# Kernel optimization log

Measured on AMD Instinct MI355X. Metric: run time of the kernel, lower is better.

Reference implementation:

```python
import jax, jax.numpy as jnp
import numpy as np

B, S, D, H = 4, 2048, 1024, 16
HD = D // H


def setup_inputs() -> dict:
    key = jax.random.key(0)
    ks = jax.random.split(key, 6)
    scale = 1.0 / np.sqrt(D)
    return {
        'x': jax.random.normal(ks[0], (B, S, D), dtype=jnp.float32),
        'wq': jax.random.normal(ks[1], (D, D), dtype=jnp.float32) * scale,
        'wk': jax.random.normal(ks[2], (D, D), dtype=jnp.float32) * scale,
        'wv': jax.random.normal(ks[3], (D, D), dtype=jnp.float32) * scale,
        'wo': jax.random.normal(ks[4], (D, D), dtype=jnp.float32) * scale,
        'wo_b': jnp.zeros((D,), dtype=jnp.float32),
    }


def reference(x, wq, wk, wv, wo, wo_b):
    b, s, _ = x.shape
    # Linear projections (torch Linear: x @ W.T), reshape to [b, h, s, hd]
    def proj(w):
        return jnp.einsum('bsd,ed->bse', x, w).reshape(b, s, H, HD).transpose(0, 2, 1, 3)
    q, k, v = proj(wq), proj(wk), proj(wv)
    scores = jnp.einsum('bhqd,bhkd->bhqk', q, k)  # [b,h,s,s]
    causal = jnp.triu(jnp.ones((s, s), dtype=bool), k=1)
    scores = jnp.where(causal, -jnp.inf, scores)
    attn = jax.nn.softmax(scores / np.sqrt(HD), axis=-1)
    ctx = jnp.einsum('bhqk,bhkd->bhqd', attn, v)  # [b,h,s,hd]
    ctx = ctx.transpose(0, 2, 1, 3).reshape(b, s, D)
    return jnp.einsum('bsd,ed->bse', ctx, wo) + wo_b
```

## Files before the change

### kernel.cpp

```cpp
#include <hip/hip_runtime.h>

#define SB 4
#define SS 2048
#define SD 1024
#define SH 16
#define SHD 64
#define SM (SB * SS)

typedef __bf16 bf16x8 __attribute__((ext_vector_type(8)));
typedef float f32x4 __attribute__((ext_vector_type(4)));

static __device__ __forceinline__ unsigned short f2bf(float x) {
    unsigned int u = __builtin_bit_cast(unsigned int, x);
    u += 0x7fffu + ((u >> 16) & 1u);
    return (unsigned short)(u >> 16);
}

static __device__ __forceinline__ float fast_exp2(float x) {
#if __has_builtin(__builtin_amdgcn_exp2f)
    return __builtin_amdgcn_exp2f(x);
#else
    return exp2f(x);
#endif
}

static __device__ __forceinline__ unsigned int pkhi(float a, float b) {
    return __builtin_amdgcn_perm(__builtin_bit_cast(unsigned int, a),
                                 __builtin_bit_cast(unsigned int, b), 0x07060302u);
}

typedef __attribute__((address_space(1))) void GV;
typedef __attribute__((address_space(3))) void LV;

static __device__ __forceinline__ void async16(const void* g, void* l) {
    __builtin_amdgcn_global_load_lds((GV*)g, (LV*)l, 16, 0, 0);
}

#define QSCALE 0.18033688011112042f

__global__ __launch_bounds__(256) void cast_all(
    const float* __restrict__ x,  const float* __restrict__ wq,
    const float* __restrict__ wk, const float* __restrict__ wv,
    const float* __restrict__ wo,
    unsigned short* __restrict__ xb, unsigned short* __restrict__ wqkv,
    unsigned short* __restrict__ wo16) {
    int base = blockIdx.x * 512 + threadIdx.x;
#pragma unroll
    for (int it = 0; it < 2; ++it) {
        int i = base + it * 256;
        const float4* src;
        ushort4* dst;
        if (i < 2097152) {
            src = reinterpret_cast<const float4*>(x) + i;
            dst = reinterpret_cast<ushort4*>(xb) + i;
        } else {
            int j = i - 2097152;
            int which = j >> 18;
            int r = j & 262143;
            if (which == 0) {
                src = reinterpret_cast<const float4*>(wq) + r;
                dst = reinterpret_cast<ushort4*>(wqkv) + r;
            } else if (which == 1) {
                src = reinterpret_cast<const float4*>(wk) + r;
                dst = reinterpret_cast<ushort4*>(wqkv) + 262144 + r;
            } else if (which == 2) {
                src = reinterpret_cast<const float4*>(wv) + r;
                dst = reinterpret_cast<ushort4*>(wqkv) + 524288 + r;
            } else {
                src = reinterpret_cast<const float4*>(wo) + r;
                dst = reinterpret_cast<ushort4*>(wo16) + r;
            }
        }
        float4 v = *src;
        ushort4 o;
        o.x = f2bf(v.x); o.y = f2bf(v.y); o.z = f2bf(v.z); o.w = f2bf(v.w);
        *dst = o;
    }
}

#define NT16 (SD / 64)

__device__ __forceinline__ void gemm_mainloop(
    const unsigned short* __restrict__ A,
    const unsigned short* __restrict__ Bt,
    int tileM, int tileN, int tid,
    unsigned short* As0, unsigned short* As1, unsigned short* As2,
    unsigned short* Bs0, unsigned short* Bs1,
    f32x4 (&acc)[4][4]) {

    const int lane = tid & 63;
    const int quad = lane >> 4;
    const int col0 = lane & 15;
    const int w = tid >> 6;
    const int wm = w >> 1;
    const int wn = w & 1;

    const int r0 = tid >> 3;
    const int cc = ((tid & 7) ^ (r0 & 7)) * 8;

    const unsigned short* gA0 = A + (size_t)(tileM + r0) * SD + cc;
    const unsigned short* gA1 = gA0 + (size_t)64 * SD;
    const unsigned short* gA2 = gA0 + (size_t)128 * SD;
    const unsigned short* gA3 = gA0 + (size_t)192 * SD;
    const unsigned short* gB0 = Bt + (size_t)(tileN + r0) * SD + cc;
    const unsigned short* gB1 = gB0 + (size_t)64 * SD;

    unsigned short* const Asb[3] = {As0, As1, As2};
    unsigned short* const Bsb[2] = {Bs0, Bs1};
    const int t16 = tid * 16;

    const int cs0 = (quad ^ (col0 & 7)) * 16;
    const int cs1 = ((4 + quad) ^ (col0 & 7)) * 16;
    const int arow = (wm * 64 + col0) * 128;
    const int brow = (wn * 64 + col0) * 128;

#define STAGE_A(t, Asx) do {                                         \
        async16(gA0 + (t) * 64, (char*)(Asx) + t16);                 \
        async16(gA1 + (t) * 64, (char*)(Asx) + 8192 + t16);          \
        async16(gA2 + (t) * 64, (char*)(Asx) + 16384 + t16);         \
        async16(gA3 + (t) * 64, (char*)(Asx) + 24576 + t16);         \
    } while (0)
#define STAGE_B(t, Bsx) do {                                         \
        async16(gB0 + (t) * 64, (char*)(Bsx) + t16);                 \
        async16(gB1 + (t) * 64, (char*)(Bsx) + 8192 + t16);          \
    } while (0)

    STAGE_A(0, As0);
    STAGE_B(0, Bs0);
    STAGE_A(1, As1);

#pragma unroll
    for (int t = 0; t < NT16; ++t) {
        if (t + 1 < NT16)
            asm volatile("s_waitcnt vmcnt(4)" ::: "memory");
        else
            asm volatile("s_waitcnt vmcnt(0)" ::: "memory");
        __builtin_amdgcn_s_barrier();
        __builtin_amdgcn_sched_barrier(0);

        const unsigned short* As = Asb[t % 3];
        const unsigned short* Bs = Bsb[t & 1];

        bf16x8 af[4][2], bfr[4][2];
#pragma unroll
        for (int fr = 0; fr < 4; ++fr) {
            const char* rp = (const char*)As + arow + fr * 2048;
            af[fr][0] = *reinterpret_cast<const bf16x8*>(rp + cs0);
            af[fr][1] = *reinterpret_cast<const bf16x8*>(rp + cs1);
        }
#pragma unroll
        for (int fc = 0; fc < 4; ++fc) {
            const char* rp = (const char*)Bs + brow + fc * 2048;
            bfr[fc][0] = *reinterpret_cast<const bf16x8*>(rp + cs0);
            bfr[fc][1] = *reinterpret_cast<const bf16x8*>(rp + cs1);
        }

        if (t + 1 < NT16) STAGE_B(t + 1, Bsb[(t + 1) & 1]);
        if (t + 2 < NT16) STAGE_A(t + 2, Asb[(t + 2) % 3]);

        __builtin_amdgcn_s_setprio(1);
#pragma unroll
        for (int ks = 0; ks < 2; ++ks)
#pragma unroll
            for (int fr = 0; fr < 4; ++fr)
#pragma unroll
                for (int fc = 0; fc < 4; ++fc)
                    acc[fr][fc] = __builtin_amdgcn_mfma_f32_16x16x32_bf16(
                        af[fr][ks], bfr[fc][ks], acc[fr][fc], 0, 0, 0);
        __builtin_amdgcn_s_setprio(0);
    }
#undef STAGE_A
#undef STAGE_B
}

__global__ __launch_bounds__(512, 2) void gemm_qkv(
    const unsigned short* __restrict__ xb,
    const unsigned short* __restrict__ wqkv,
    unsigned short* __restrict__ Qd,
    unsigned short* __restrict__ Kd,
    unsigned short* __restrict__ Vtd) {

    __shared__ __align__(16) unsigned short As0[256 * 64];
    __shared__ __align__(16) unsigned short As1[256 * 64];
    __shared__ __align__(16) unsigned short As2[256 * 64];
    __shared__ __align__(16) unsigned short Bs0[128 * 64];
    __shared__ __align__(16) unsigned short Bs1[128 * 64];
    const int tid = threadIdx.x;
    const int tileN = blockIdx.x * 128;
    const int tileM = blockIdx.y * 256;

    f32x4 acc[4][4];
    const f32x4 z = {0.f, 0.f, 0.f, 0.f};
#pragma unroll
    for (int i = 0; i < 4; ++i)
#pragma unroll
        for (int j = 0; j < 4; ++j) acc[i][j] = z;

    gemm_mainloop(xb, wqkv, tileM, tileN, tid, As0, As1, As2, Bs0, Bs1, acc);

    const int lane = tid & 63, quad = lane >> 4, col0 = lane & 15;
    const int w = tid >> 6, wm = w >> 1, wn = w & 1;

#pragma unroll
    for (int ct = 0; ct < 4; ++ct) {
        int n0 = tileN + wn * 64 + ct * 16;
        int which = n0 >> 10;
        int e0 = n0 & 1023;
        int h = e0 >> 6;
        int hd = (e0 & 63) + col0;
#pragma unroll
        for (int rt = 0; rt < 4; ++rt) {
            int m0 = tileM + wm * 64 + rt * 16 + quad * 4;
            int bb = m0 >> 11;
            int s0 = m0 & 2047;
            int bh = bb * SH + h;
            if (which == 0) {
                int base = (bh * SS + s0) * SHD + hd;
#pragma unroll
                for (int r = 0; r < 4; ++r)
                    Qd[base + r * SHD] = f2bf(acc[rt][ct][r] * QSCALE);
            } else if (which == 1) {
                int base = (bh * SS + s0) * SHD + hd;
#pragma unroll
                for (int r = 0; r < 4; ++r)
                    Kd[base + r * SHD] = f2bf(acc[rt][ct][r]);
            } else {
                int base = (bh * SHD + hd) * SS + s0;
                ushort4 pk;
                pk.x = f2bf(acc[rt][ct][0]);
                pk.y = f2bf(acc[rt][ct][1]);
                pk.z = f2bf(acc[rt][ct][2]);
                pk.w = f2bf(acc[rt][ct][3]);
                *reinterpret_cast<ushort4*>(Vtd + base) = pk;
            }
        }
    }
}

__global__ __launch_bounds__(512, 2) void gemm_out(
    const unsigned short* __restrict__ ctx,
    const unsigned short* __restrict__ wo16,
    const float* __restrict__ wb,
    float* __restrict__ out) {

    __shared__ __align__(16) unsigned short As0[256 * 64];
    __shared__ __align__(16) unsigned short As1[256 * 64];
    __shared__ __align__(16) unsigned short As2[256 * 64];
    __shared__ __align__(16) unsigned short Bs0[128 * 64];
    __shared__ __align__(16) unsigned short Bs1[128 * 64];
    const int tid = threadIdx.x;
    const int tileN = blockIdx.x * 128;
    const int tileM = blockIdx.y * 256;

    f32x4 acc[4][4];
    const f32x4 z = {0.f, 0.f, 0.f, 0.f};
#pragma unroll
    for (int i = 0; i < 4; ++i)
#pragma unroll
        for (int j = 0; j < 4; ++j) acc[i][j] = z;

    gemm_mainloop(ctx, wo16, tileM, tileN, tid, As0, As1, As2, Bs0, Bs1, acc);

    const int lane = tid & 63, quad = lane >> 4, col0 = lane & 15;
    const int w = tid >> 6, wm = w >> 1, wn = w & 1;

#pragma unroll
    for (int ct = 0; ct < 4; ++ct) {
        int n = tileN + wn * 64 + ct * 16 + col0;
        float bias = wb[n];
#pragma unroll
        for (int rt = 0; rt < 4; ++rt) {
            int m0 = tileM + wm * 64 + rt * 16 + quad * 4;
#pragma unroll
            for (int r = 0; r < 4; ++r)
                out[(size_t)(m0 + r) * SD + n] = acc[rt][ct][r] + bias;
        }
    }
}

#define PSTR 72

__device__ __forceinline__ void stage_kv(
    const unsigned short* __restrict__ Kg,
    const unsigned short* __restrict__ Vtg,
    size_t base, int t, int srow0, int scs, int tid,
    unsigned short* Kb, unsigned short* Vb) {
#pragma unroll
    for (int j = 0; j < 2; ++j) {
        int row = j * 32 + srow0;
        int chunk = scs ^ (row & 7);
        int slot16 = (j * 256 + tid) * 16;
        async16(Kg + base + (size_t)(t * 64 + row) * SHD + chunk * 8,
                (char*)Kb + slot16);
        async16(Vtg + base + (size_t)row * SS + t * 64 + chunk * 8,
                (char*)Vb + slot16);
    }
}

__device__ __forceinline__ void attn_tile(
    const unsigned short* __restrict__ Kc,
    const unsigned short* __restrict__ Vc,
    int kb, int q0, int quad, int col0,
    const bf16x8 (&bq)[2][2], const bf16x8& ones,
    unsigned short* Psw, f32x4 (&ot)[2][4], f32x4 (&lacc)[2]) {

    const f32x4 z = {0.f, 0.f, 0.f, 0.f};

    bf16x8 ak[4][2];
#pragma unroll
    for (int rt = 0; rt < 4; ++rt)
#pragma unroll
        for (int ks = 0; ks < 2; ++ks)
            ak[rt][ks] = *reinterpret_cast<const bf16x8*>(
                &Kc[(rt * 16 + col0) * 64 + ((ks * 4 + quad) ^ (col0 & 7)) * 8]);

    f32x4 sc[2][4];
#pragma unroll
    for (int g = 0; g < 2; ++g)
#pragma unroll
        for (int rt = 0; rt < 4; ++rt) sc[g][rt] = z;
    __builtin_amdgcn_s_setprio(1);
#pragma unroll
    for (int rt = 0; rt < 4; ++rt)
#pragma unroll
        for (int g = 0; g < 2; ++g) {
            sc[g][rt] = __builtin_amdgcn_mfma_f32_16x16x32_bf16(
                ak[rt][0], bq[g][0], sc[g][rt], 0, 0, 0);
            sc[g][rt] = __builtin_amdgcn_mfma_f32_16x16x32_bf16(
                ak[rt][1], bq[g][1], sc[g][rt], 0, 0, 0);
        }
    __builtin_amdgcn_s_setprio(0);

    if (kb + 63 > q0) {
#pragma unroll
        for (int g = 0; g < 2; ++g) {
            int q = q0 + g * 16 + col0;
#pragma unroll
            for (int rt = 0; rt < 4; ++rt)
#pragma unroll
                for (int r = 0; r < 4; ++r) {
                    int key = kb + rt * 16 + quad * 4 + r;
                    if (key > q) sc[g][rt][r] = -3.0e38f;
                }
        }
    }

#pragma unroll
    for (int g = 0; g < 2; ++g)
#pragma unroll
        for (int rt = 0; rt < 4; ++rt)
#pragma unroll
            for (int r = 0; r < 4; ++r)
                sc[g][rt][r] = fast_exp2(sc[g][rt][r]);

    bf16x8 bp[2][2];
#pragma unroll
    for (int g = 0; g < 2; ++g) {
#pragma unroll
        for (int rt = 0; rt < 4; ++rt) {
            uint2 pk;
            pk.x = pkhi(sc[g][rt][1], sc[g][rt][0]);
            pk.y = pkhi(sc[g][rt][3], sc[g][rt][2]);
            *reinterpret_cast<uint2*>(&Psw[col0 * PSTR + rt * 16 + quad * 4]) = pk;
        }
#pragma unroll
        for (int ks = 0; ks < 2; ++ks)
            bp[g][ks] = *reinterpret_cast<const bf16x8*>(
                &Psw[col0 * PSTR + ks * 32 + quad * 8]);
    }

    __builtin_amdgcn_s_setprio(1);
#pragma unroll
    for (int ks = 0; ks < 2; ++ks) {
        lacc[0] = __builtin_amdgcn_mfma_f32_16x16x32_bf16(ones, bp[0][ks], lacc[0], 0, 0, 0);
        lacc[1] = __builtin_amdgcn_mfma_f32_16x16x32_bf16(ones, bp[1][ks], lacc[1], 0, 0, 0);
#pragma unroll
        for (int ct = 0; ct < 4; ++ct) {
            bf16x8 av = *reinterpret_cast<const bf16x8*>(
                &Vc[(ct * 16 + col0) * 64 + ((ks * 4 + quad) ^ (col0 & 7)) * 8]);
            ot[0][ct] = __builtin_amdgcn_mfma_f32_16x16x32_bf16(av, bp[0][ks], ot[0][ct], 0, 0, 0);
            ot[1][ct] = __builtin_amdgcn_mfma_f32_16x16x32_bf16(av, bp[1][ks], ot[1][ct], 0, 0, 0);
        }
    }
    __builtin_amdgcn_s_setprio(0);
}

__device__ __forceinline__ void attn_pass(
    const unsigned short* __restrict__ Qg,
    const unsigned short* __restrict__ Kg,
    const unsigned short* __restrict__ Vtg,
    unsigned short* __restrict__ ctx,
    size_t base, int b, int h, int jj,
    int tid, int w, int quad, int col0,
    unsigned short* K0, unsigned short* K1, unsigned short* K2, unsigned short* K3,
    unsigned short* V0, unsigned short* V1, unsigned short* V2, unsigned short* V3,
    unsigned short* Psw, const bf16x8& ones) {

    const int q0 = jj * 128 + w * 32;
    const int qlim = q0 + 31;

    bf16x8 bq[2][2];
#pragma unroll
    for (int g = 0; g < 2; ++g)
#pragma unroll
        for (int ks = 0; ks < 2; ++ks)
            bq[g][ks] = *reinterpret_cast<const bf16x8*>(
                Qg + base + (size_t)(q0 + g * 16 + col0) * SHD + ks * 32 + quad * 8);

    f32x4 ot[2][4], lacc[2];
    const f32x4 z = {0.f, 0.f, 0.f, 0.f};
#pragma unroll
    for (int g = 0; g < 2; ++g) {
        lacc[g] = z;
#pragma unroll
        for (int ct = 0; ct < 4; ++ct) ot[g][ct] = z;
    }

    const int srow0 = tid >> 3;
    const int scs = tid & 7;
    const int nkt = 2 * jj + 2;

    __syncthreads();
    stage_kv(Kg, Vtg, base, 0, srow0, scs, tid, K0, V0);
    if (1 < nkt) stage_kv(Kg, Vtg, base, 1, srow0, scs, tid, K1, V1);

#pragma unroll 1
    for (int kt = 0; kt < nkt; kt += 4) {
        __syncthreads();
        if (kt + 2 < nkt) stage_kv(Kg, Vtg, base, kt + 2, srow0, scs, tid, K2, V2);
        if (kt + 3 < nkt) stage_kv(Kg, Vtg, base, kt + 3, srow0, scs, tid, K3, V3);
        if (kt * 64 <= qlim)
            attn_tile(K0, V0, kt * 64, q0, quad, col0, bq, ones, Psw, ot, lacc);
        if ((kt + 1) * 64 <= qlim)
            attn_tile(K1, V1, (kt + 1) * 64, q0, quad, col0, bq, ones, Psw, ot, lacc);

        if (kt + 2 >= nkt) break;
        __syncthreads();
        if (kt + 4 < nkt) stage_kv(Kg, Vtg, base, kt + 4, srow0, scs, tid, K0, V0);
        if (kt + 5 < nkt) stage_kv(Kg, Vtg, base, kt + 5, srow0, scs, tid, K1, V1);
        if ((kt + 2) * 64 <= qlim)
            attn_tile(K2, V2, (kt + 2) * 64, q0, quad, col0, bq, ones, Psw, ot, lacc);
        if (kt + 3 < nkt && (kt + 3) * 64 <= qlim)
            attn_tile(K3, V3, (kt + 3) * 64, q0, quad, col0, bq, ones, Psw, ot, lacc);
    }

#pragma unroll
    for (int g = 0; g < 2; ++g) {
        float inv = 1.0f / lacc[g][0];
        int q = q0 + g * 16 + col0;
        size_t obase = ((size_t)b * SS + q) * SD + h * SHD;
#pragma unroll
        for (int ct = 0; ct < 4; ++ct) {
            uint2 pk;
            pk.x = pkhi(ot[g][ct][1] * inv, ot[g][ct][0] * inv);
            pk.y = pkhi(ot[g][ct][3] * inv, ot[g][ct][2] * inv);
            *reinterpret_cast<uint2*>(ctx + obase + ct * 16 + quad * 4) = pk;
        }
    }
}

__global__ __launch_bounds__(256) void attn_kernel(
    const unsigned short* __restrict__ Qg,
    const unsigned short* __restrict__ Kg,
    const unsigned short* __restrict__ Vtg,
    unsigned short* __restrict__ ctx) {

    __shared__ __align__(16) unsigned short K0[64 * 64];
    __shared__ __align__(16) unsigned short K1[64 * 64];
    __shared__ __align__(16) unsigned short K2[64 * 64];
    __shared__ __align__(16) unsigned short K3[64 * 64];
    __shared__ __align__(16) unsigned short V0[64 * 64];
    __shared__ __align__(16) unsigned short V1[64 * 64];
    __shared__ __align__(16) unsigned short V2[64 * 64];
    __shared__ __align__(16) unsigned short V3[64 * 64];
    __shared__ __align__(16) unsigned short Ps[4 * 16 * PSTR];

    const int tid = threadIdx.x;
    const int w = tid >> 6;
    const int lane = tid & 63;
    const int quad = lane >> 4;
    const int col0 = lane & 15;

    const int bh = (blockIdx.x << 3) | (blockIdx.y & 7);
    const int jx = blockIdx.y >> 3;

    const int b = bh >> 4;
    const int h = bh & 15;
    const size_t base = (size_t)bh * (SS * SHD);
    unsigned short* Psw = Ps + w * 16 * PSTR;

    bf16x8 ones;
#pragma unroll
    for (int i = 0; i < 8; ++i) ones[i] = (__bf16)1.0f;

    attn_pass(Qg, Kg, Vtg, ctx, base, b, h, jx,
              tid, w, quad, col0, K0, K1, K2, K3, V0, V1, V2, V3, Psw, ones);
    attn_pass(Qg, Kg, Vtg, ctx, base, b, h, 15 - jx,
              tid, w, quad, col0, K0, K1, K2, K3, V0, V1, V2, V3, Psw, ones);
}

extern "C" void kernel_launch(void* const* d_in, const int* in_sizes, int n_in,
                              void* d_out, int out_size, void* d_ws, size_t ws_size,
                              hipStream_t stream) {
    const float* x  = (const float*)d_in[0];
    const float* wq = (const float*)d_in[1];
    const float* wk = (const float*)d_in[2];
    const float* wv = (const float*)d_in[3];
    const float* wo = (const float*)d_in[4];
    const float* wb = (const float*)d_in[5];
    float* out = (float*)d_out;

    char* ws = (char*)d_ws;
    unsigned short* xb   = (unsigned short*)(ws + 0);
    unsigned short* wqkv = (unsigned short*)(ws + 16777216);
    unsigned short* q    = (unsigned short*)(ws + 23068672);
    unsigned short* k    = (unsigned short*)(ws + 39845888);
    unsigned short* vt   = (unsigned short*)(ws + 56623104);
    unsigned short* ctx  = (unsigned short*)(ws + 73400320);
    unsigned short* wo16 = (unsigned short*)(ws + 90177536);

    cast_all<<<6144, 256, 0, stream>>>(x, wq, wk, wv, wo, xb, wqkv, wo16);

    gemm_qkv<<<dim3(3 * SD / 128, SM / 256), 512, 0, stream>>>(xb, wqkv, q, k, vt);

    attn_kernel<<<dim3(8, SB * SH), 256, 0, stream>>>(q, k, vt, ctx);

    gemm_out<<<dim3(SD / 128, SM / 256), 512, 0, stream>>>(ctx, wo16, wb, out);
}
```

Measured before the change: 234.6 us.

## Merge paired causal query blocks into one K/V sweep sharing staged tiles

Previously each block made two separate passes over K/V, one for the low query block jj and one for the mirrored block 15-jj, and restaged the shared K/V prefix each time. Now a single sweep processes both query blocks together. Each K/V tile is loaded to LDS once and reused for both query sets, with the low block masked off once it is past its causal limit. This halves K/V staging traffic and barriers for the shared prefix, but doubles accumulator registers per thread. The kernel also now asks for 2 blocks per CU through launch_bounds, which may force register spills. Both P tiles are written to the same per-warp Psw buffer, which relies on the B-side LDS write being ordered after the A-side reads.

```diff
diff --git a/kernel.cpp b/kernel.cpp
--- a/kernel.cpp
+++ b/kernel.cpp
@@ -297,44 +297,33 @@
     }
 }
 
-__device__ __forceinline__ void attn_tile(
-    const unsigned short* __restrict__ Kc,
-    const unsigned short* __restrict__ Vc,
-    int kb, int q0, int quad, int col0,
-    const bf16x8 (&bq)[2][2], const bf16x8& ones,
-    unsigned short* Psw, f32x4 (&ot)[2][4], f32x4 (&lacc)[2]) {
+__device__ __forceinline__ void qk_softmax_pair(
+    const bf16x8 (&ak)[4][2], const bf16x8& bq0, const bf16x8& bq1,
+    const bf16x8& bq0b, const bf16x8& bq1b,
+    int kb, int qrow0, int quad, int col0,
+    unsigned short* Psw, bf16x8 (&bp)[2][2]) {
 
     const f32x4 z = {0.f, 0.f, 0.f, 0.f};
-
-    bf16x8 ak[4][2];
-#pragma unroll
-    for (int rt = 0; rt < 4; ++rt)
-#pragma unroll
-        for (int ks = 0; ks < 2; ++ks)
-            ak[rt][ks] = *reinterpret_cast<const bf16x8*>(
-                &Kc[(rt * 16 + col0) * 64 + ((ks * 4 + quad) ^ (col0 & 7)) * 8]);
-
     f32x4 sc[2][4];
 #pragma unroll
     for (int g = 0; g < 2; ++g)
 #pragma unroll
         for (int rt = 0; rt < 4; ++rt) sc[g][rt] = z;
+
     __builtin_amdgcn_s_setprio(1);
 #pragma unroll
-    for (int rt = 0; rt < 4; ++rt)
+    for (int rt = 0; rt < 4; ++rt) {
+        sc[0][rt] = __builtin_amdgcn_mfma_f32_16x16x32_bf16(ak[rt][0], bq0, sc[0][rt], 0, 0, 0);
+        sc[1][rt] = __builtin_amdgcn_mfma_f32_16x16x32_bf16(ak[rt][0], bq0b, sc[1][rt], 0, 0, 0);
+        sc[0][rt] = __builtin_amdgcn_mfma_f32_16x16x32_bf16(ak[rt][1], bq1, sc[0][rt], 0, 0, 0);
+        sc[1][rt] = __builtin_amdgcn_mfma_f32_16x16x32_bf16(ak[rt][1], bq1b, sc[1][rt], 0, 0, 0);
+    }
+    __builtin_amdgcn_s_setprio(0);
+
+    if (kb + 63 > qrow0) {
 #pragma unroll
         for (int g = 0; g < 2; ++g) {
-            sc[g][rt] = __builtin_amdgcn_mfma_f32_16x16x32_bf16(
-                ak[rt][0], bq[g][0], sc[g][rt], 0, 0, 0);
-            sc[g][rt] = __builtin_amdgcn_mfma_f32_16x16x32_bf16(
-                ak[rt][1], bq[g][1], sc[g][rt], 0, 0, 0);
-        }
-    __builtin_amdgcn_s_setprio(0);
-
-    if (kb + 63 > q0) {
-#pragma unroll
-        for (int g = 0; g < 2; ++g) {
-            int q = q0 + g * 16 + col0;
+            int q = qrow0 + g * 16 + col0;
 #pragma unroll
             for (int rt = 0; rt < 4; ++rt)
 #pragma unroll
@@ -353,7 +342,6 @@
             for (int r = 0; r < 4; ++r)
                 sc[g][rt][r] = fast_exp2(sc[g][rt][r]);
 
-    bf16x8 bp[2][2];
 #pragma unroll
     for (int g = 0; g < 2; ++g) {
 #pragma unroll
@@ -368,98 +356,57 @@
             bp[g][ks] = *reinterpret_cast<const bf16x8*>(
                 &Psw[col0 * PSTR + ks * 32 + quad * 8]);
     }
+}
+
+__device__ __forceinline__ void attn_tile9(
+    const unsigned short* __restrict__ Kc,
+    const unsigned short* __restrict__ Vc,
+    int kb, int qlimA, int q0a, int q0b, int quad, int col0,
+    const bf16x8 (&bq)[4][2], const bf16x8& ones,
+    unsigned short* Psw, f32x4 (&ot)[4][4], f32x4 (&lacc)[4]) {
+
+    bf16x8 ak[4][2];
+#pragma unroll
+    for (int rt = 0; rt < 4; ++rt)
+#pragma unroll
+        for (int ks = 0; ks < 2; ++ks)
+            ak[rt][ks] = *reinterpret_cast<const bf16x8*>(
+                &Kc[(rt * 16 + col0) * 64 + ((ks * 4 + quad) ^ (col0 & 7)) * 8]);
+
+    const bool actA = (kb <= qlimA);
+
+    bf16x8 bpA[2][2], bpB[2][2];
+    if (actA)
+        qk_softmax_pair(ak, bq[0][0], bq[0][1], bq[1][0], bq[1][1],
+                        kb, q0a, quad, col0, Psw, bpA);
+    qk_softmax_pair(ak, bq[2][0], bq[2][1], bq[3][0], bq[3][1],
+                    kb, q0b, quad, col0, Psw, bpB);
 
     __builtin_amdgcn_s_setprio(1);
 #pragma unroll
     for (int ks = 0; ks < 2; ++ks) {
-        lacc[0] = __builtin_amdgcn_mfma_f32_16x16x32_bf16(ones, bp[0][ks], lacc[0], 0, 0, 0);
-        lacc[1] = __builtin_amdgcn_mfma_f32_16x16x32_bf16(ones, bp[1][ks], lacc[1], 0, 0, 0);
+        lacc[2] = __builtin_amdgcn_mfma_f32_16x16x32_bf16(ones, bpB[0][ks], lacc[2], 0, 0, 0);
+        lacc[3] = __builtin_amdgcn_mfma_f32_16x16x32_bf16(ones, bpB[1][ks], lacc[3], 0, 0, 0);
+        if (actA) {
+            lacc[0] = __builtin_amdgcn_mfma_f32_16x16x32_bf16(ones, bpA[0][ks], lacc[0], 0, 0, 0);
+            lacc[1] = __builtin_amdgcn_mfma_f32_16x16x32_bf16(ones, bpA[1][ks], lacc[1], 0, 0, 0);
+        }
 #pragma unroll
         for (int ct = 0; ct < 4; ++ct) {
             bf16x8 av = *reinterpret_cast<const bf16x8*>(
                 &Vc[(ct * 16 + col0) * 64 + ((ks * 4 + quad) ^ (col0 & 7)) * 8]);
-            ot[0][ct] = __builtin_amdgcn_mfma_f32_16x16x32_bf16(av, bp[0][ks], ot[0][ct], 0, 0, 0);
-            ot[1][ct] = __builtin_amdgcn_mfma_f32_16x16x32_bf16(av, bp[1][ks], ot[1][ct], 0, 0, 0);
+            ot[2][ct] = __builtin_amdgcn_mfma_f32_16x16x32_bf16(av, bpB[0][ks], ot[2][ct], 0, 0, 0);
+            ot[3][ct] = __builtin_amdgcn_mfma_f32_16x16x32_bf16(av, bpB[1][ks], ot[3][ct], 0, 0, 0);
+            if (actA) {
+                ot[0][ct] = __builtin_amdgcn_mfma_f32_16x16x32_bf16(av, bpA[0][ks], ot[0][ct], 0, 0, 0);
+                ot[1][ct] = __builtin_amdgcn_mfma_f32_16x16x32_bf16(av, bpA[1][ks], ot[1][ct], 0, 0, 0);
+            }
         }
     }
     __builtin_amdgcn_s_setprio(0);
 }
 
-__device__ __forceinline__ void attn_pass(
-    const unsigned short* __restrict__ Qg,
-    const unsigned short* __restrict__ Kg,
-    const unsigned short* __restrict__ Vtg,
-    unsigned short* __restrict__ ctx,
-    size_t base, int b, int h, int jj,
-    int tid, int w, int quad, int col0,
-    unsigned short* K0, unsigned short* K1, unsigned short* K2, unsigned short* K3,
-    unsigned short* V0, unsigned short* V1, unsigned short* V2, unsigned short* V3,
-    unsigned short* Psw, const bf16x8& ones) {
-
-    const int q0 = jj * 128 + w * 32;
-    const int qlim = q0 + 31;
-
-    bf16x8 bq[2][2];
-#pragma unroll
-    for (int g = 0; g < 2; ++g)
-#pragma unroll
-        for (int ks = 0; ks < 2; ++ks)
-            bq[g][ks] = *reinterpret_cast<const bf16x8*>(
-                Qg + base + (size_t)(q0 + g * 16 + col0) * SHD + ks * 32 + quad * 8);
-
-    f32x4 ot[2][4], lacc[2];
-    const f32x4 z = {0.f, 0.f, 0.f, 0.f};
-#pragma unroll
-    for (int g = 0; g < 2; ++g) {
-        lacc[g] = z;
-#pragma unroll
-        for (int ct = 0; ct < 4; ++ct) ot[g][ct] = z;
-    }
-
-    const int srow0 = tid >> 3;
-    const int scs = tid & 7;
-    const int nkt = 2 * jj + 2;
-
-    __syncthreads();
-    stage_kv(Kg, Vtg, base, 0, srow0, scs, tid, K0, V0);
-    if (1 < nkt) stage_kv(Kg, Vtg, base, 1, srow0, scs, tid, K1, V1);
-
-#pragma unroll 1
-    for (int kt = 0; kt < nkt; kt += 4) {
-        __syncthreads();
-        if (kt + 2 < nkt) stage_kv(Kg, Vtg, base, kt + 2, srow0, scs, tid, K2, V2);
-        if (kt + 3 < nkt) stage_kv(Kg, Vtg, base, kt + 3, srow0, scs, tid, K3, V3);
-        if (kt * 64 <= qlim)
-            attn_tile(K0, V0, kt * 64, q0, quad, col0, bq, ones, Psw, ot, lacc);
-        if ((kt + 1) * 64 <= qlim)
-            attn_tile(K1, V1, (kt + 1) * 64, q0, quad, col0, bq, ones, Psw, ot, lacc);
-
-        if (kt + 2 >= nkt) break;
-        __syncthreads();
-        if (kt + 4 < nkt) stage_kv(Kg, Vtg, base, kt + 4, srow0, scs, tid, K0, V0);
-        if (kt + 5 < nkt) stage_kv(Kg, Vtg, base, kt + 5, srow0, scs, tid, K1, V1);
-        if ((kt + 2) * 64 <= qlim)
-            attn_tile(K2, V2, (kt + 2) * 64, q0, quad, col0, bq, ones, Psw, ot, lacc);
-        if (kt + 3 < nkt && (kt + 3) * 64 <= qlim)
-            attn_tile(K3, V3, (kt + 3) * 64, q0, quad, col0, bq, ones, Psw, ot, lacc);
-    }
-
-#pragma unroll
-    for (int g = 0; g < 2; ++g) {
-        float inv = 1.0f / lacc[g][0];
-        int q = q0 + g * 16 + col0;
-        size_t obase = ((size_t)b * SS + q) * SD + h * SHD;
-#pragma unroll
-        for (int ct = 0; ct < 4; ++ct) {
-            uint2 pk;
-            pk.x = pkhi(ot[g][ct][1] * inv, ot[g][ct][0] * inv);
-            pk.y = pkhi(ot[g][ct][3] * inv, ot[g][ct][2] * inv);
-            *reinterpret_cast<uint2*>(ctx + obase + ct * 16 + quad * 4) = pk;
-        }
-    }
-}
-
-__global__ __launch_bounds__(256) void attn_kernel(
+__global__ __launch_bounds__(256, 2) void attn_kernel(
     const unsigned short* __restrict__ Qg,
     const unsigned short* __restrict__ Kg,
     const unsigned short* __restrict__ Vtg,
@@ -482,7 +429,7 @@
     const int col0 = lane & 15;
 
     const int bh = (blockIdx.x << 3) | (blockIdx.y & 7);
-    const int jx = blockIdx.y >> 3;
+    const int jj = blockIdx.y >> 3;
 
     const int b = bh >> 4;
     const int h = bh & 15;
@@ -493,10 +440,74 @@
 #pragma unroll
     for (int i = 0; i < 8; ++i) ones[i] = (__bf16)1.0f;
 
-    attn_pass(Qg, Kg, Vtg, ctx, base, b, h, jx,
-              tid, w, quad, col0, K0, K1, K2, K3, V0, V1, V2, V3, Psw, ones);
-    attn_pass(Qg, Kg, Vtg, ctx, base, b, h, 15 - jx,
-              tid, w, quad, col0, K0, K1, K2, K3, V0, V1, V2, V3, Psw, ones);
+    const int q0a = jj * 128 + w * 32;
+    const int q0b = (15 - jj) * 128 + w * 32;
+    const int qlimA = q0a + 31;
+    const int qlimB = q0b + 31;
+    const int nkt = 32 - 2 * jj;
+
+    bf16x8 bq[4][2];
+#pragma unroll
+    for (int g = 0; g < 4; ++g) {
+        int qr = (g < 2 ? q0a + g * 16 : q0b + (g - 2) * 16) + col0;
+#pragma unroll
+        for (int ks = 0; ks < 2; ++ks)
+            bq[g][ks] = *reinterpret_cast<const bf16x8*>(
+                Qg + base + (size_t)qr * SHD + ks * 32 + quad * 8);
+    }
+
+    f32x4 ot[4][4], lacc[4];
+    const f32x4 z = {0.f, 0.f, 0.f, 0.f};
+#pragma unroll
+    for (int g = 0; g < 4; ++g) {
+        lacc[g] = z;
+#pragma unroll
+        for (int ct = 0; ct < 4; ++ct) ot[g][ct] = z;
+    }
+
+    const int srow0 = tid >> 3;
+    const int scs = tid & 7;
+
+    stage_kv(Kg, Vtg, base, 0, srow0, scs, tid, K0, V0);
+    stage_kv(Kg, Vtg, base, 1, srow0, scs, tid, K1, V1);
+
+#pragma unroll 1
+    for (int kt = 0; kt < nkt; kt += 4) {
+        __syncthreads();
+        if (kt + 2 < nkt) stage_kv(Kg, Vtg, base, kt + 2, srow0, scs, tid, K2, V2);
+        if (kt + 3 < nkt) stage_kv(Kg, Vtg, base, kt + 3, srow0, scs, tid, K3, V3);
+        if (kt * 64 <= qlimB)
+            attn_tile9(K0, V0, kt * 64, qlimA, q0a, q0b, quad, col0,
+                       bq, ones, Psw, ot, lacc);
+        if ((kt + 1) * 64 <= qlimB)
+            attn_tile9(K1, V1, (kt + 1) * 64, qlimA, q0a, q0b, quad, col0,
+                       bq, ones, Psw, ot, lacc);
+
+        if (kt + 2 >= nkt) break;
+        __syncthreads();
+        if (kt + 4 < nkt) stage_kv(Kg, Vtg, base, kt + 4, srow0, scs, tid, K0, V0);
+        if (kt + 5 < nkt) stage_kv(Kg, Vtg, base, kt + 5, srow0, scs, tid, K1, V1);
+        if ((kt + 2) * 64 <= qlimB)
+            attn_tile9(K2, V2, (kt + 2) * 64, qlimA, q0a, q0b, quad, col0,
+                       bq, ones, Psw, ot, lacc);
+        if ((kt + 3) < nkt && (kt + 3) * 64 <= qlimB)
+            attn_tile9(K3, V3, (kt + 3) * 64, qlimA, q0a, q0b, quad, col0,
+                       bq, ones, Psw, ot, lacc);
+    }
+
+#pragma unroll
+    for (int g = 0; g < 4; ++g) {
+        float inv = 1.0f / lacc[g][0];
+        int q = (g < 2 ? q0a + g * 16 : q0b + (g - 2) * 16) + col0;
+        size_t obase = ((size_t)b * SS + q) * SD + h * SHD;
+#pragma unroll
+        for (int ct = 0; ct < 4; ++ct) {
+            uint2 pk;
+            pk.x = pkhi(ot[g][ct][1] * inv, ot[g][ct][0] * inv);
+            pk.y = pkhi(ot[g][ct][3] * inv, ot[g][ct][2] * inv);
+            *reinterpret_cast<uint2*>(ctx + obase + ct * 16 + quad * 4) = pk;
+        }
+    }
 }
 
 extern "C" void kernel_launch(void* const* d_in, const int* in_sizes, int n_in,
```

Measured after the change: 235.2 us. No clear change (+0.3%).

## Split causal attention into one query tile per block with double-buffered K/V

Applied to the files above, without the earlier changes.

The attention kernel now launches twice as many blocks, each handling a single 128-row query tile. Previously each block processed a balanced pair of tiles (jx and 15-jx) in sequence. Tiles are ordered heaviest-first through the j2 = 15 - index mapping, and the K/V staging ring drops from four buffers to two, with one tile prefetched ahead. This roughly halves LDS use per block, which should allow more resident blocks per CU and finer-grained load balancing. The cost is a shallower prefetch pipeline that may expose more global-load latency, plus per-block tail imbalance from causal work varying between tiles.

```diff
diff --git a/kernel.cpp b/kernel.cpp
--- a/kernel.cpp
+++ b/kernel.cpp
@@ -385,19 +385,39 @@
     __builtin_amdgcn_s_setprio(0);
 }
 
-__device__ __forceinline__ void attn_pass(
+__global__ __launch_bounds__(256) void attn_kernel(
     const unsigned short* __restrict__ Qg,
     const unsigned short* __restrict__ Kg,
     const unsigned short* __restrict__ Vtg,
-    unsigned short* __restrict__ ctx,
-    size_t base, int b, int h, int jj,
-    int tid, int w, int quad, int col0,
-    unsigned short* K0, unsigned short* K1, unsigned short* K2, unsigned short* K3,
-    unsigned short* V0, unsigned short* V1, unsigned short* V2, unsigned short* V3,
-    unsigned short* Psw, const bf16x8& ones) {
-
-    const int q0 = jj * 128 + w * 32;
+    unsigned short* __restrict__ ctx) {
+
+    __shared__ __align__(16) unsigned short K0[64 * 64];
+    __shared__ __align__(16) unsigned short K1[64 * 64];
+    __shared__ __align__(16) unsigned short V0[64 * 64];
+    __shared__ __align__(16) unsigned short V1[64 * 64];
+    __shared__ __align__(16) unsigned short Ps[4 * 16 * PSTR];
+
+    const int tid = threadIdx.x;
+    const int w = tid >> 6;
+    const int lane = tid & 63;
+    const int quad = lane >> 4;
+    const int col0 = lane & 15;
+
+    const int bh = (blockIdx.x << 3) | (blockIdx.y & 7);
+    const int j2 = 15 - (blockIdx.y >> 3);
+
+    const int b = bh >> 4;
+    const int h = bh & 15;
+    const size_t base = (size_t)bh * (SS * SHD);
+    unsigned short* Psw = Ps + w * 16 * PSTR;
+
+    bf16x8 ones;
+#pragma unroll
+    for (int i = 0; i < 8; ++i) ones[i] = (__bf16)1.0f;
+
+    const int q0 = j2 * 128 + w * 32;
     const int qlim = q0 + 31;
+    const int nkt = 2 * j2 + 2;
 
     bf16x8 bq[2][2];
 #pragma unroll
@@ -418,30 +438,21 @@
 
     const int srow0 = tid >> 3;
     const int scs = tid & 7;
-    const int nkt = 2 * jj + 2;
-
-    __syncthreads();
+
     stage_kv(Kg, Vtg, base, 0, srow0, scs, tid, K0, V0);
-    if (1 < nkt) stage_kv(Kg, Vtg, base, 1, srow0, scs, tid, K1, V1);
 
 #pragma unroll 1
-    for (int kt = 0; kt < nkt; kt += 4) {
+    for (int kt = 0; kt < nkt; ++kt) {
         __syncthreads();
-        if (kt + 2 < nkt) stage_kv(Kg, Vtg, base, kt + 2, srow0, scs, tid, K2, V2);
-        if (kt + 3 < nkt) stage_kv(Kg, Vtg, base, kt + 3, srow0, scs, tid, K3, V3);
-        if (kt * 64 <= qlim)
-            attn_tile(K0, V0, kt * 64, q0, quad, col0, bq, ones, Psw, ot, lacc);
-        if ((kt + 1) * 64 <= qlim)
-            attn_tile(K1, V1, (kt + 1) * 64, q0, quad, col0, bq, ones, Psw, ot, lacc);
-
-        if (kt + 2 >= nkt) break;
-        __syncthreads();
-        if (kt + 4 < nkt) stage_kv(Kg, Vtg, base, kt + 4, srow0, scs, tid, K0, V0);
-        if (kt + 5 < nkt) stage_kv(Kg, Vtg, base, kt + 5, srow0, scs, tid, K1, V1);
-        if ((kt + 2) * 64 <= qlim)
-            attn_tile(K2, V2, (kt + 2) * 64, q0, quad, col0, bq, ones, Psw, ot, lacc);
-        if (kt + 3 < nkt && (kt + 3) * 64 <= qlim)
-            attn_tile(K3, V3, (kt + 3) * 64, q0, quad, col0, bq, ones, Psw, ot, lacc);
+        if (kt + 1 < nkt) {
+            if (kt & 1) stage_kv(Kg, Vtg, base, kt + 1, srow0, scs, tid, K0, V0);
+            else        stage_kv(Kg, Vtg, base, kt + 1, srow0, scs, tid, K1, V1);
+        }
+        if (kt * 64 <= qlim) {
+            const unsigned short* Kc = (kt & 1) ? K1 : K0;
+            const unsigned short* Vc = (kt & 1) ? V1 : V0;
+            attn_tile(Kc, Vc, kt * 64, q0, quad, col0, bq, ones, Psw, ot, lacc);
+        }
     }
 
 #pragma unroll
@@ -457,46 +468,6 @@
             *reinterpret_cast<uint2*>(ctx + obase + ct * 16 + quad * 4) = pk;
         }
     }
-}
-
-__global__ __launch_bounds__(256) void attn_kernel(
-    const unsigned short* __restrict__ Qg,
-    const unsigned short* __restrict__ Kg,
-    const unsigned short* __restrict__ Vtg,
-    unsigned short* __restrict__ ctx) {
-
-    __shared__ __align__(16) unsigned short K0[64 * 64];
-    __shared__ __align__(16) unsigned short K1[64 * 64];
-    __shared__ __align__(16) unsigned short K2[64 * 64];
-    __shared__ __align__(16) unsigned short K3[64 * 64];
-    __shared__ __align__(16) unsigned short V0[64 * 64];
-    __shared__ __align__(16) unsigned short V1[64 * 64];
-    __shared__ __align__(16) unsigned short V2[64 * 64];
-    __shared__ __align__(16) unsigned short V3[64 * 64];
-    __shared__ __align__(16) unsigned short Ps[4 * 16 * PSTR];
-
-    const int tid = threadIdx.x;
-    const int w = tid >> 6;
-    const int lane = tid & 63;
-    const int quad = lane >> 4;
-    const int col0 = lane & 15;
-
-    const int bh = (blockIdx.x << 3) | (blockIdx.y & 7);
-    const int jx = blockIdx.y >> 3;
-
-    const int b = bh >> 4;
-    const int h = bh & 15;
-    const size_t base = (size_t)bh * (SS * SHD);
-    unsigned short* Psw = Ps + w * 16 * PSTR;
-
-    bf16x8 ones;
-#pragma unroll
-    for (int i = 0; i < 8; ++i) ones[i] = (__bf16)1.0f;
-
-    attn_pass(Qg, Kg, Vtg, ctx, base, b, h, jx,
-              tid, w, quad, col0, K0, K1, K2, K3, V0, V1, V2, V3, Psw, ones);
-    attn_pass(Qg, Kg, Vtg, ctx, base, b, h, 15 - jx,
-              tid, w, quad, col0, K0, K1, K2, K3, V0, V1, V2, V3, Psw, ones);
 }
 
 extern "C" void kernel_launch(void* const* d_in, const int* in_sizes, int n_in,
@@ -523,7 +494,7 @@
 
     gemm_qkv<<<dim3(3 * SD / 128, SM / 256), 512, 0, stream>>>(xb, wqkv, q, k, vt);
 
-    attn_kernel<<<dim3(8, SB * SH), 256, 0, stream>>>(q, k, vt, ctx);
+    attn_kernel<<<dim3(8, 2 * SB * SH), 256, 0, stream>>>(q, k, vt, ctx);
 
     gemm_out<<<dim3(SD / 128, SM / 256), 512, 0, stream>>>(ctx, wo16, wb, out);
 }
```

After: 242.2 us. 1.03x slower.
